# Performance work log

Hardware: AMD Instinct MI355X
Metric: run time of the kernel (lower is better)

Reference implementation:

```python
import jax, jax.numpy as jnp
import numpy as np

N_NODES = 50000
N_EDGES = 800000
D = 64
B = 64
HL = 128  # lstm hidden
OUT = 32


def setup_inputs() -> dict:
    key = jax.random.key(0)
    ks = jax.random.split(key, 16)
    s = 0.05
    return {
        "x": jax.random.normal(ks[0], (N_NODES, D), jnp.float32),
        "edge_index": jax.random.randint(ks[1], (2, N_EDGES), 0, N_NODES),
        "batch": jnp.sort(jax.random.randint(ks[2], (N_NODES,), 0, B)),
        "w1": jax.random.normal(ks[3], (D, D), jnp.float32) * s,
        "b1": jnp.zeros((D,), jnp.float32),
        "w2": jax.random.normal(ks[4], (D, D), jnp.float32) * s,
        "b2": jnp.zeros((D,), jnp.float32),
        "w3": jax.random.normal(ks[5], (D, D), jnp.float32) * s,
        "b3": jnp.zeros((D,), jnp.float32),
        "w4": jax.random.normal(ks[6], (D, D), jnp.float32) * s,
        "b4": jnp.zeros((D,), jnp.float32),
        "w_ih": jax.random.normal(ks[7], (4 * HL, D), jnp.float32) * s,
        "w_hh": jax.random.normal(ks[8], (4 * HL, HL), jnp.float32) * s,
        "b_ih": jnp.zeros((4 * HL,), jnp.float32),
        "b_hh": jnp.zeros((4 * HL,), jnp.float32),
        "fc_w": jax.random.normal(ks[9], (OUT, HL), jnp.float32) * s,
        "fc_b": jnp.zeros((OUT,), jnp.float32),
        "h0": jax.random.normal(ks[10], (1, B, HL), jnp.float32),
        "c0": jax.random.normal(ks[11], (1, B, HL), jnp.float32),
    }


def _gin(x, edge_index, wA, bA, wB, bB):
    # GINConv with eps=0: MLP(x + sum_{j->i} x_j); scatter-add over edges
    agg = jax.ops.segment_sum(x[edge_index[0]], edge_index[1], num_segments=N_NODES)
    h = x + agg
    h = jax.nn.relu(h @ wA.T + bA)
    return h @ wB.T + bB


def reference(x, edge_index, batch, w1, b1, w2, b2, w3, b3, w4, b4,
              w_ih, w_hh, b_ih, b_hh, fc_w, fc_b, h0, c0):
    h = jax.nn.relu(_gin(x, edge_index, w1, b1, w2, b2))  # dropout = identity (eval)
    h = jax.nn.relu(_gin(h, edge_index, w3, b3, w4, b4))
    # global_mean_pool over graphs
    sums = jax.ops.segment_sum(h, batch, num_segments=B)              # [B, D]
    cnts = jax.ops.segment_sum(jnp.ones((N_NODES,), h.dtype), batch, num_segments=B)
    pooled = sums / jnp.maximum(cnts, 1.0)[:, None]
    # single-step LSTM (PyTorch gate order: i, f, g, o)
    gates = pooled @ w_ih.T + b_ih + h0[0] @ w_hh.T + b_hh            # [B, 4H]
    i, f, g, o = jnp.split(gates, 4, axis=-1)
    c1 = jax.nn.sigmoid(f) * c0[0] + jax.nn.sigmoid(i) * jnp.tanh(g)
    h1 = jax.nn.sigmoid(o) * jnp.tanh(c1)
    logits = h1 @ fc_w.T + fc_b
    probs = jax.nn.softmax(logits, axis=1)
    return probs, h1[None], c1[None]
```

## Files before the change

### kernel.cpp

```cpp
#include <hip/hip_runtime.h>
#include <hip/hip_bf16.h>

#define N_NODES 50000
#define N_EDGES 800000
#define D 64
#define B 64
#define HL 128
#define OUT 32

#define CAP 64
#define STP 72
#define PK 8

#define BINS 196
#define EPB 2048
#define LCAP 48
#define BCAP 4608

typedef __attribute__((ext_vector_type(8))) short          short8;
typedef __attribute__((ext_vector_type(8))) unsigned short ushort8_t;
typedef __attribute__((ext_vector_type(4))) float          floatx4;

__device__ __forceinline__ unsigned short f2bf(float f)
{
    unsigned u = __float_as_uint(f);
    u = (u + 0x7FFFu + ((u >> 16) & 1u)) >> 16;
    return (unsigned short)u;
}
__device__ __forceinline__ float bf2f(unsigned short s)
{
    return __uint_as_float(((unsigned)s) << 16);
}

__global__ __launch_bounds__(256) void cvt_kernel(
    const float* __restrict__ x, unsigned short* __restrict__ xb,
    const float* __restrict__ w1, const float* __restrict__ w2,
    const float* __restrict__ w3, const float* __restrict__ w4,
    unsigned short* __restrict__ wb)
{
    int i = blockIdx.x * 256 + threadIdx.x;
    const float4 v = reinterpret_cast<const float4*>(x)[i];
    ushort4 o;
    o.x = f2bf(v.x); o.y = f2bf(v.y); o.z = f2bf(v.z); o.w = f2bf(v.w);
    reinterpret_cast<ushort4*>(xb)[i] = o;

    if (blockIdx.x < 64) {
        int j = blockIdx.x * 256 + threadIdx.x;
        int m = j >> 12, off = j & 4095;
        const float* src = (m == 0) ? w1 : (m == 1) ? w2 : (m == 2) ? w3 : w4;
        wb[j] = f2bf(src[off]);
    }
}

__global__ __launch_bounds__(256) void binA_kernel(
    const int* __restrict__ ei, int* __restrict__ bincnt,
    unsigned* __restrict__ binbuf)
{
    __shared__ int      lcnt[BINS];
    __shared__ int      gbase[BINS];
    __shared__ unsigned lbuf[BINS * LCAP];

    int t = threadIdx.x;
    if (t < BINS) lcnt[t] = 0;
    __syncthreads();

    int base = blockIdx.x * EPB;
#pragma unroll
    for (int i = 0; i < EPB / 256; ++i) {
        int e = base + i * 256 + t;
        if (e < N_EDGES) {
            int s = ei[e];
            int d = ei[N_EDGES + e];
            int bin = d >> 8;
            unsigned pk = (unsigned)s | ((unsigned)(d & 255) << 16);
            int p = atomicAdd(&lcnt[bin], 1);
            if (p < LCAP) {
                lbuf[bin * LCAP + p] = pk;
            } else {
                int q = atomicAdd(&bincnt[bin], 1);
                if (q < BCAP) binbuf[bin * BCAP + q] = pk;
            }
        }
    }
    __syncthreads();

    if (t < BINS) {
        int m = lcnt[t]; m = (m < LCAP) ? m : LCAP;
        gbase[t] = (m > 0) ? atomicAdd(&bincnt[t], m) : 0;
    }
    __syncthreads();

    int wv = t >> 6, lane = t & 63;
    for (int b = wv; b < BINS; b += 4) {
        int m = lcnt[b]; m = (m < LCAP) ? m : LCAP;
        int gb = gbase[b];
        for (int j = lane; j < m; j += 64)
            if (gb + j < BCAP) binbuf[b * BCAP + gb + j] = lbuf[b * LCAP + j];
    }
}

__global__ __launch_bounds__(256) void binB_kernel(
    const int*      __restrict__ bincnt,
    const unsigned* __restrict__ binbuf,
    int*            __restrict__ cnt,
    unsigned short* __restrict__ bucket)
{
    __shared__ int            lc[256];
    __shared__ unsigned short lbkt[256 * CAP];

    int t = threadIdx.x;
    lc[t] = 0;
    __syncthreads();

    int bin = blockIdx.x;
    int m = bincnt[bin]; m = (m < BCAP) ? m : BCAP;
    const unsigned* src = binbuf + bin * BCAP;
    for (int j = t; j < m; j += 256) {
        unsigned pk = src[j];
        int dlow = (pk >> 16) & 255;
        int p = atomicAdd(&lc[dlow], 1);
        if (p < CAP) lbkt[dlow * CAP + p] = (unsigned short)(pk & 0xFFFFu);
    }
    __syncthreads();

    int n0 = bin * 256;
    int n = n0 + t;
    if (n < N_NODES) cnt[n] = (lc[t] < CAP) ? lc[t] : CAP;

    for (int idx = t; idx < 256 * 8; idx += 256) {
        int r = idx >> 3, c = idx & 7;
        if (n0 + r < N_NODES)
            *reinterpret_cast<ushort8_t*>(
                bucket + (size_t)(n0 + r) * CAP + c * 8) =
                *reinterpret_cast<const ushort8_t*>(&lbkt[r * CAP + c * 8]);
    }
}

__global__ __launch_bounds__(256) void gather_kernel(
    const unsigned short* __restrict__ feat,
    const int*            __restrict__ cnt,
    const unsigned short* __restrict__ bucket,
    unsigned short*       __restrict__ outp)
{
    int wv = threadIdx.x >> 6, lane = threadIdx.x & 63;
    int n = blockIdx.x * 4 + wv;
    if (n >= N_NODES) return;

    int deg = cnt[n];
    deg = (deg < CAP) ? deg : CAP;
    const unsigned short* bkt = bucket + (size_t)n * CAP;

    float acc = bf2f(feat[(size_t)n * D + lane]);
    int e = 0;
    for (; e + 8 <= deg; e += 8) {
        ushort8_t ia = *reinterpret_cast<const ushort8_t*>(bkt + e);
        float v0 = bf2f(feat[(size_t)ia[0] * D + lane]);
        float v1 = bf2f(feat[(size_t)ia[1] * D + lane]);
        float v2 = bf2f(feat[(size_t)ia[2] * D + lane]);
        float v3 = bf2f(feat[(size_t)ia[3] * D + lane]);
        float v4 = bf2f(feat[(size_t)ia[4] * D + lane]);
        float v5 = bf2f(feat[(size_t)ia[5] * D + lane]);
        float v6 = bf2f(feat[(size_t)ia[6] * D + lane]);
        float v7 = bf2f(feat[(size_t)ia[7] * D + lane]);
        acc += ((v0 + v1) + (v2 + v3)) + ((v4 + v5) + (v6 + v7));
    }
    for (; e + 4 <= deg; e += 4) {
        ushort4 ia = *reinterpret_cast<const ushort4*>(bkt + e);
        float v0 = bf2f(feat[(size_t)ia.x * D + lane]);
        float v1 = bf2f(feat[(size_t)ia.y * D + lane]);
        float v2 = bf2f(feat[(size_t)ia.z * D + lane]);
        float v3 = bf2f(feat[(size_t)ia.w * D + lane]);
        acc += (v0 + v1) + (v2 + v3);
    }
    for (; e < deg; ++e) acc += bf2f(feat[(size_t)bkt[e] * D + lane]);

    outp[(size_t)n * D + lane] = f2bf(acc);
}

__global__ __launch_bounds__(256) void mlp_kernel(
    const unsigned short* __restrict__ feat,
    const unsigned short* __restrict__ wAb,
    const float*          __restrict__ bA,
    const unsigned short* __restrict__ wBb,
    const float*          __restrict__ bB,
    unsigned short*       __restrict__ outp)
{
    __shared__ __align__(16) unsigned short st[4][16 * STP];

    const int wv   = threadIdx.x >> 6;
    const int lane = threadIdx.x & 63;
    const int quad = lane >> 4;
    const int col  = lane & 15;

    const int n0 = (blockIdx.x * 4 + wv) * 16;
    if (n0 >= N_NODES) return;

    float bAl[4], bBl[4];
#pragma unroll
    for (int t = 0; t < 4; ++t) {
        bAl[t] = bA[t * 16 + col];
        bBl[t] = bB[t * 16 + col];
    }

    short8 WA[4][2], WB[4][2];
#pragma unroll
    for (int t = 0; t < 4; ++t)
#pragma unroll
        for (int k = 0; k < 2; ++k) {
            WA[t][k] = *reinterpret_cast<const short8*>(
                wAb + (t * 16 + col) * D + k * 32 + quad * 8);
            WB[t][k] = *reinterpret_cast<const short8*>(
                wBb + (t * 16 + col) * D + k * 32 + quad * 8);
        }

    short8 A0 = *reinterpret_cast<const short8*>(
        feat + (size_t)(n0 + col) * D + 0 * 32 + quad * 8);
    short8 A1 = *reinterpret_cast<const short8*>(
        feat + (size_t)(n0 + col) * D + 1 * 32 + quad * 8);

    unsigned short* stw = &st[wv][0];

#pragma unroll
    for (int t = 0; t < 4; ++t) {
        floatx4 c = {0.0f, 0.0f, 0.0f, 0.0f};
        c = __builtin_amdgcn_mfma_f32_16x16x32_bf16(A0, WA[t][0], c, 0, 0, 0);
        c = __builtin_amdgcn_mfma_f32_16x16x32_bf16(A1, WA[t][1], c, 0, 0, 0);
#pragma unroll
        for (int r = 0; r < 4; ++r) {
            float v = fmaxf(c[r] + bAl[t], 0.0f);
            stw[(quad * 4 + r) * STP + t * 16 + col] = f2bf(v);
        }
    }

    short8 T0 = *reinterpret_cast<const short8*>(stw + col * STP + 0 * 32 + quad * 8);
    short8 T1 = *reinterpret_cast<const short8*>(stw + col * STP + 1 * 32 + quad * 8);

#pragma unroll
    for (int t = 0; t < 4; ++t) {
        floatx4 c = {0.0f, 0.0f, 0.0f, 0.0f};
        c = __builtin_amdgcn_mfma_f32_16x16x32_bf16(T0, WB[t][0], c, 0, 0, 0);
        c = __builtin_amdgcn_mfma_f32_16x16x32_bf16(T1, WB[t][1], c, 0, 0, 0);
#pragma unroll
        for (int r = 0; r < 4; ++r) {
            float v = fmaxf(c[r] + bBl[t], 0.0f);
            outp[(size_t)(n0 + quad * 4 + r) * D + t * 16 + col] = f2bf(v);
        }
    }
}

__device__ __forceinline__ int lower_bound_dev(const int* a, int n, int v)
{
    int lo = 0, hi = n;
    while (lo < hi) {
        int m = (lo + hi) >> 1;
        if (a[m] < v) lo = m + 1; else hi = m;
    }
    return lo;
}

__global__ __launch_bounds__(256) void pool_partial_kernel(
    const unsigned short* __restrict__ feat,
    const int*            __restrict__ batch,
    float*                __restrict__ psum)
{
    int b = blockIdx.x >> 3;
    int k = blockIdx.x & (PK - 1);
    int start = lower_bound_dev(batch, N_NODES, b);
    int end   = lower_bound_dev(batch, N_NODES, b + 1);

    int d = threadIdx.x & 63;
    int r = threadIdx.x >> 6;

    float acc = 0.0f;
    for (int n = start + k * 4 + r; n < end; n += PK * 4)
        acc += bf2f(feat[(size_t)n * D + d]);

    __shared__ float red[4][D];
    red[r][d] = acc;
    __syncthreads();
    if (r == 0)
        psum[((size_t)b * PK + k) * D + d] =
            red[0][d] + red[1][d] + red[2][d] + red[3][d];
}

__device__ __forceinline__ float sigmoidf_(float x) { return 1.0f / (1.0f + expf(-x)); }

__global__ __launch_bounds__(512) void head_kernel(
    const float* __restrict__ psum,
    const int*   __restrict__ batch,
    const float* __restrict__ w_ih,
    const float* __restrict__ w_hh,
    const float* __restrict__ b_ih,
    const float* __restrict__ b_hh,
    const float* __restrict__ fc_w,
    const float* __restrict__ fc_b,
    const float* __restrict__ h0,
    const float* __restrict__ c0,
    float*       __restrict__ out_probs,
    float*       __restrict__ out_h1,
    float*       __restrict__ out_c1)
{
    int b = blockIdx.x;
    int j = threadIdx.x;

    __shared__ float sp[D];
    __shared__ float sh[HL];
    __shared__ float gates[4 * HL];
    __shared__ float sh1[HL];
    __shared__ float slog[OUT];

    if (j < D) {
        int start = lower_bound_dev(batch, N_NODES, b);
        int end   = lower_bound_dev(batch, N_NODES, b + 1);
        float s = 0.0f;
#pragma unroll
        for (int k = 0; k < PK; ++k) s += psum[((size_t)b * PK + k) * D + j];
        sp[j] = s / fmaxf((float)(end - start), 1.0f);
    } else if (j < D + HL) {
        sh[j - D] = h0[b * HL + (j - D)];
    }
    __syncthreads();

    {
        float acc = b_ih[j] + b_hh[j];
#pragma unroll
        for (int k = 0; k < D; ++k)  acc = fmaf(sp[k], w_ih[j * D + k], acc);
#pragma unroll
        for (int k = 0; k < HL; ++k) acc = fmaf(sh[k], w_hh[j * HL + k], acc);
        gates[j] = acc;
    }
    __syncthreads();

    if (j < HL) {
        float ig = gates[j];
        float fg = gates[HL + j];
        float gg = gates[2 * HL + j];
        float og = gates[3 * HL + j];
        float c  = sigmoidf_(fg) * c0[b * HL + j] + sigmoidf_(ig) * tanhf(gg);
        float hv = sigmoidf_(og) * tanhf(c);
        out_c1[b * HL + j] = c;
        out_h1[b * HL + j] = hv;
        sh1[j] = hv;
    }
    __syncthreads();

    if (j < OUT) {
        float a = fc_b[j];
#pragma unroll
        for (int k = 0; k < HL; ++k) a = fmaf(sh1[k], fc_w[j * HL + k], a);
        slog[j] = a;
    }
    __syncthreads();

    if (j < OUT) {
        float m = -1e30f;
#pragma unroll
        for (int k = 0; k < OUT; ++k) m = fmaxf(m, slog[k]);
        float s = 0.0f;
#pragma unroll
        for (int k = 0; k < OUT; ++k) s += expf(slog[k] - m);
        out_probs[b * OUT + j] = expf(slog[j] - m) / s;
    }
}

extern "C" void kernel_launch(void* const* d_in, const int* in_sizes, int n_in,
                              void* d_out, int out_size, void* d_ws, size_t ws_size,
                              hipStream_t stream)
{
    const float* x     = (const float*)d_in[0];
    const int*   ei    = (const int*)  d_in[1];
    const int*   batch = (const int*)  d_in[2];
    const float* w1    = (const float*)d_in[3];
    const float* b1    = (const float*)d_in[4];
    const float* w2    = (const float*)d_in[5];
    const float* b2    = (const float*)d_in[6];
    const float* w3    = (const float*)d_in[7];
    const float* b3    = (const float*)d_in[8];
    const float* w4    = (const float*)d_in[9];
    const float* b4    = (const float*)d_in[10];
    const float* w_ih  = (const float*)d_in[11];
    const float* w_hh  = (const float*)d_in[12];
    const float* b_ih  = (const float*)d_in[13];
    const float* b_hh  = (const float*)d_in[14];
    const float* fc_w  = (const float*)d_in[15];
    const float* fc_b  = (const float*)d_in[16];
    const float* h0    = (const float*)d_in[17];
    const float* c0    = (const float*)d_in[18];

    int* bincnt = (int*)d_ws;
    int* cnt    = bincnt + 256;
    unsigned* binbuf = (unsigned*)(cnt + N_NODES);
    unsigned short* bucket = (unsigned short*)(binbuf + (size_t)BINS * BCAP);
    unsigned short* xb = bucket + (size_t)N_NODES * CAP;
    unsigned short* g  = xb + (size_t)N_NODES * D;
    unsigned short* h1 = g  + (size_t)N_NODES * D;
    unsigned short* wb = h1 + (size_t)N_NODES * D;
    float* psum = (float*)(wb + 4 * D * D);

    float* out_probs = (float*)d_out;
    float* out_h1    = out_probs + B * OUT;
    float* out_c1    = out_h1 + B * HL;

    const int cb = N_NODES * D / 4 / 256;
    const int ab = (N_EDGES + EPB - 1) / EPB;
    const int gb = N_NODES / 4;
    const int mb = (N_NODES / 16 + 3) / 4;

    cvt_kernel<<<cb, 256, 0, stream>>>(x, xb, w1, w2, w3, w4, wb);

    hipMemsetAsync(bincnt, 0, 256 * sizeof(int), stream);
    binA_kernel<<<ab, 256, 0, stream>>>(ei, bincnt, binbuf);
    binB_kernel<<<BINS, 256, 0, stream>>>(bincnt, binbuf, cnt, bucket);

    gather_kernel<<<gb, 256, 0, stream>>>(xb, cnt, bucket, g);
    mlp_kernel<<<mb, 256, 0, stream>>>(g, wb, b1, wb + 4096, b2, h1);

    gather_kernel<<<gb, 256, 0, stream>>>(h1, cnt, bucket, g);
    mlp_kernel<<<mb, 256, 0, stream>>>(g, wb + 8192, b3, wb + 12288, b4, xb);

    pool_partial_kernel<<<B * PK, 256, 0, stream>>>(xb, batch, psum);
    head_kernel<<<B, 512, 0, stream>>>(psum, batch, w_ih, w_hh, b_ih, b_hh,
                                       fc_w, fc_b, h0, c0,
                                       out_probs, out_h1, out_c1);
}
```

Baseline: 237.2 us.

## Pad neighbor buckets with a zero row and gather in fixed 16-wide rounds

Bucket slots past each node's degree are pre-filled with the index of an extra all-zero feature row, so the gather kernel can read neighbors in uniform 16-wide rounds with no remainder loops. This gives more independent loads in flight per iteration and removes divergent tail handling. The hipMemsetAsync is folded into the conversion kernel, which also zeroes the padding rows. In exchange, up to 15 wasted loads per node hit the zero row, and the workspace layout grows by 16 rows per feature buffer.

```diff
diff --git a/kernel.cpp b/kernel.cpp
--- a/kernel.cpp
+++ b/kernel.cpp
@@ -11,6 +11,7 @@
 #define CAP 64
 #define STP 72
 #define PK 8
+#define ZROW N_NODES
 
 #define BINS 196
 #define EPB 2048
@@ -36,7 +37,9 @@
     const float* __restrict__ x, unsigned short* __restrict__ xb,
     const float* __restrict__ w1, const float* __restrict__ w2,
     const float* __restrict__ w3, const float* __restrict__ w4,
-    unsigned short* __restrict__ wb)
+    unsigned short* __restrict__ wb,
+    int* __restrict__ bincnt,
+    unsigned short* __restrict__ g, unsigned short* __restrict__ h1)
 {
     int i = blockIdx.x * 256 + threadIdx.x;
     const float4 v = reinterpret_cast<const float4*>(x)[i];
@@ -49,6 +52,16 @@
         int m = j >> 12, off = j & 4095;
         const float* src = (m == 0) ? w1 : (m == 1) ? w2 : (m == 2) ? w3 : w4;
         wb[j] = f2bf(src[off]);
+    }
+
+    if (blockIdx.x == 64) {
+        int t = threadIdx.x;
+        bincnt[t] = 0;
+        if (t < D) {
+            xb[(size_t)ZROW * D + t] = 0;
+            g [(size_t)ZROW * D + t] = 0;
+            h1[(size_t)ZROW * D + t] = 0;
+        }
     }
 }
 
@@ -110,6 +123,11 @@
 
     int t = threadIdx.x;
     lc[t] = 0;
+    {
+        ushort8_t fill = {ZROW, ZROW, ZROW, ZROW, ZROW, ZROW, ZROW, ZROW};
+        for (int idx = t; idx < 256 * CAP / 8; idx += 256)
+            reinterpret_cast<ushort8_t*>(lbkt)[idx] = fill;
+    }
     __syncthreads();
 
     int bin = blockIdx.x;
@@ -144,16 +162,16 @@
 {
     int wv = threadIdx.x >> 6, lane = threadIdx.x & 63;
     int n = blockIdx.x * 4 + wv;
-    if (n >= N_NODES) return;
 
     int deg = cnt[n];
     deg = (deg < CAP) ? deg : CAP;
+    int rounds = (deg + 15) >> 4;
     const unsigned short* bkt = bucket + (size_t)n * CAP;
 
     float acc = bf2f(feat[(size_t)n * D + lane]);
-    int e = 0;
-    for (; e + 8 <= deg; e += 8) {
-        ushort8_t ia = *reinterpret_cast<const ushort8_t*>(bkt + e);
+    for (int r = 0; r < rounds; ++r) {
+        ushort8_t ia = *reinterpret_cast<const ushort8_t*>(bkt + r * 16);
+        ushort8_t ib = *reinterpret_cast<const ushort8_t*>(bkt + r * 16 + 8);
         float v0 = bf2f(feat[(size_t)ia[0] * D + lane]);
         float v1 = bf2f(feat[(size_t)ia[1] * D + lane]);
         float v2 = bf2f(feat[(size_t)ia[2] * D + lane]);
@@ -162,18 +180,17 @@
         float v5 = bf2f(feat[(size_t)ia[5] * D + lane]);
         float v6 = bf2f(feat[(size_t)ia[6] * D + lane]);
         float v7 = bf2f(feat[(size_t)ia[7] * D + lane]);
-        acc += ((v0 + v1) + (v2 + v3)) + ((v4 + v5) + (v6 + v7));
-    }
-    for (; e + 4 <= deg; e += 4) {
-        ushort4 ia = *reinterpret_cast<const ushort4*>(bkt + e);
-        float v0 = bf2f(feat[(size_t)ia.x * D + lane]);
-        float v1 = bf2f(feat[(size_t)ia.y * D + lane]);
-        float v2 = bf2f(feat[(size_t)ia.z * D + lane]);
-        float v3 = bf2f(feat[(size_t)ia.w * D + lane]);
-        acc += (v0 + v1) + (v2 + v3);
-    }
-    for (; e < deg; ++e) acc += bf2f(feat[(size_t)bkt[e] * D + lane]);
-
+        float v8 = bf2f(feat[(size_t)ib[0] * D + lane]);
+        float v9 = bf2f(feat[(size_t)ib[1] * D + lane]);
+        float va = bf2f(feat[(size_t)ib[2] * D + lane]);
+        float vb = bf2f(feat[(size_t)ib[3] * D + lane]);
+        float vc = bf2f(feat[(size_t)ib[4] * D + lane]);
+        float vd = bf2f(feat[(size_t)ib[5] * D + lane]);
+        float ve = bf2f(feat[(size_t)ib[6] * D + lane]);
+        float vf = bf2f(feat[(size_t)ib[7] * D + lane]);
+        acc += (((v0 + v1) + (v2 + v3)) + ((v4 + v5) + (v6 + v7)))
+             + (((v8 + v9) + (va + vb)) + ((vc + vd) + (ve + vf)));
+    }
     outp[(size_t)n * D + lane] = f2bf(acc);
 }
 
@@ -387,14 +404,15 @@
     const float* h0    = (const float*)d_in[17];
     const float* c0    = (const float*)d_in[18];
 
+    const size_t NR = (size_t)N_NODES + 16;
     int* bincnt = (int*)d_ws;
     int* cnt    = bincnt + 256;
     unsigned* binbuf = (unsigned*)(cnt + N_NODES);
     unsigned short* bucket = (unsigned short*)(binbuf + (size_t)BINS * BCAP);
     unsigned short* xb = bucket + (size_t)N_NODES * CAP;
-    unsigned short* g  = xb + (size_t)N_NODES * D;
-    unsigned short* h1 = g  + (size_t)N_NODES * D;
-    unsigned short* wb = h1 + (size_t)N_NODES * D;
+    unsigned short* g  = xb + NR * D;
+    unsigned short* h1 = g  + NR * D;
+    unsigned short* wb = h1 + NR * D;
     float* psum = (float*)(wb + 4 * D * D);
 
     float* out_probs = (float*)d_out;
@@ -406,9 +424,8 @@
     const int gb = N_NODES / 4;
     const int mb = (N_NODES / 16 + 3) / 4;
 
-    cvt_kernel<<<cb, 256, 0, stream>>>(x, xb, w1, w2, w3, w4, wb);
-
-    hipMemsetAsync(bincnt, 0, 256 * sizeof(int), stream);
+    cvt_kernel<<<cb, 256, 0, stream>>>(x, xb, w1, w2, w3, w4, wb, bincnt, g, h1);
+
     binA_kernel<<<ab, 256, 0, stream>>>(ei, bincnt, binbuf);
     binB_kernel<<<BINS, 256, 0, stream>>>(bincnt, binbuf, cnt, bucket);
 
```

Result: faster. 224.0 us (-5.6%).
